# Kernel tuning notes

Hardware: AMD Instinct MI355X
Metric: run time of the kernel (lower is better)

Reference implementation:

```python
import jax, jax.numpy as jnp
import numpy as np

DT = 0.01
T, D_IN, D_STATE = 262144, 64, 128

def setup_inputs() -> dict:
    key = jax.random.key(0)
    k1, k2, k3, k4 = jax.random.split(key, 4)
    U = jax.random.normal(k1, (T, D_IN), dtype=jnp.float32)
    A_log = jax.random.normal(k2, (D_STATE,), dtype=jnp.float32) * 0.1 - 1.0
    B = jax.random.normal(k3, (D_STATE, D_IN), dtype=jnp.float32) * 0.1
    C = jax.random.normal(k4, (D_IN, D_STATE), dtype=jnp.float32) * 0.1
    Dm = jnp.zeros((D_IN, D_IN), dtype=jnp.float32)
    h0 = jnp.zeros((D_STATE,), dtype=jnp.float32)
    return {"U": U, "A_log": A_log, "B": B, "C": C, "D": Dm, "h0": h0}

def reference(U, A_log, B, C, D, h0):
    # Discretized diagonal transition: A_disc = exp(A_log * dt)
    A_d = jnp.exp(A_log * DT)  # (d_state,)
    Bu = U @ B.T               # (T, d_state), precompute all input injections
    Du = U @ D.T               # (T, d_input)

    def step(h, bu):
        h_new = A_d * h + bu
        return h_new, h_new

    h_final, H = jax.lax.scan(step, h0, Bu)  # H: (T, d_state)
    Y = H @ C.T + Du                          # (T, d_input)
    return Y, h_final
```

## Files before the change

### kernel.cpp

```cpp
#include <hip/hip_runtime.h>


#define TT   262144
#define DIN  64
#define DS   128
#define DTC  0.01f
#define L    128
#define NG   (TT / L)
#define SEGL 16
#define NSEG (NG / SEGL)

typedef short  s8v  __attribute__((ext_vector_type(8)));
typedef float  f4v  __attribute__((ext_vector_type(4)));

__device__ __forceinline__ unsigned short f2bf(float f) {
    unsigned u = __float_as_uint(f);
    u += 0x7fffu + ((u >> 16) & 1u);
    return (unsigned short)(u >> 16);
}

__device__ __forceinline__ s8v pack8(float4 a, float4 b) {
    union { unsigned short u[8]; s8v v; } r;
    r.u[0] = f2bf(a.x); r.u[1] = f2bf(a.y); r.u[2] = f2bf(a.z); r.u[3] = f2bf(a.w);
    r.u[4] = f2bf(b.x); r.u[5] = f2bf(b.y); r.u[6] = f2bf(b.z); r.u[7] = f2bf(b.w);
    return r.v;
}

__device__ __forceinline__ const s8v* afrag(const unsigned short* sA,
                                            int mt, int ks, int q, int m) {
    int slot = (mt * 2 + ks) * 64 + (q << 4) + (m ^ (q << 2) ^ ks);
    return (const s8v*)&sA[slot * 8];
}

__device__ __forceinline__ void stage_U(const float* __restrict__ Ug,
                                        unsigned short* __restrict__ sA,
                                        int tid) {
    #pragma unroll
    for (int p = 0; p < 2; ++p) {
        int u  = tid + p * 512;
        int mt = u >> 7, ks = (u >> 6) & 1, q = (u >> 4) & 3, lo = u & 15;
        int m  = lo ^ (q << 2) ^ ks;
        const float4* gp = (const float4*)(Ug + (mt * 16 + m) * DIN + ks * 32 + q * 8);
        *(s8v*)&sA[u * 8] = pack8(gp[0], gp[1]);
    }
}

__device__ __forceinline__ s8v load_bfrag(const float* __restrict__ M,
                                          int row, int k0, int ld) {
    const float4* p = (const float4*)(M + row * ld + k0);
    return pack8(p[0], p[1]);
}

__global__ __launch_bounds__(512, 8) void ssm_k1(
    const float* __restrict__ U, const float* __restrict__ Alog,
    const float* __restrict__ B, float* __restrict__ agg,
    float* __restrict__ segAgg)
{
    __shared__ __align__(16) unsigned short sA[8192];
    const int g    = blockIdx.x;
    const int tid  = threadIdx.x;
    const int lane = tid & 63;
    const int w    = tid >> 6;
    const int q    = lane >> 4, m = lane & 15;
    const int s    = 16 * w + m;

    stage_U(U + (size_t)g * L * DIN, sA, tid);

    s8v Bf[2];
    #pragma unroll
    for (int ks = 0; ks < 2; ++ks)
        Bf[ks] = load_bfrag(B, s, ks * 32 + q * 8, DIN);

    const float cA   = Alog[s] * DTC;
    const float aInv = __expf(-cA);
    __syncthreads();

    float wsum = 0.f;
    #pragma unroll
    for (int mt = 0; mt < 8; ++mt) {
        f4v acc = (f4v){0.f, 0.f, 0.f, 0.f};
        #pragma unroll
        for (int ks = 0; ks < 2; ++ks)
            acc = __builtin_amdgcn_mfma_f32_16x16x32_bf16(*afrag(sA, mt, ks, q, m), Bf[ks], acc, 0, 0, 0);
        float wb = __expf(cA * (float)(L - 1 - (mt * 16 + q * 4)));
        #pragma unroll
        for (int r = 0; r < 4; ++r) {
            wsum = fmaf(wb, acc[r], wsum);
            if (r < 3) wb *= aInv;
        }
    }
    wsum += __shfl_xor(wsum, 16, 64);
    wsum += __shfl_xor(wsum, 32, 64);

    if (q == 0) {
        agg[(size_t)g * DS + s] = wsum;
        float wgt = __expf(cA * (float)(L * (SEGL - 1 - (g & (SEGL - 1)))));
        atomicAdd(&segAgg[(g >> 4) * DS + s], wsum * wgt);
    }
}

__global__ void ssm_k2(const float* __restrict__ Alog, const float* __restrict__ h0,
                       const float* __restrict__ segAgg, float* __restrict__ segCarry,
                       float* __restrict__ hfin)
{
    const int s = threadIdx.x;
    const float aSeg = __expf(Alog[s] * (DTC * L * SEGL));
    float c = h0[s];
    #pragma unroll 8
    for (int sg = 0; sg < NSEG; ++sg) {
        segCarry[sg * DS + s] = c;
        c = fmaf(aSeg, c, segAgg[sg * DS + s]);
    }
    hfin[s] = c;
}

__global__ __launch_bounds__(512, 6) void ssm_k3(
    const float* __restrict__ U, const float* __restrict__ Alog,
    const float* __restrict__ B, const float* __restrict__ C,
    const float* __restrict__ Dm, const float* __restrict__ agg,
    const float* __restrict__ segCarry, float* __restrict__ Y)
{
    __shared__ __align__(16) unsigned short sA[8192];
    __shared__ __align__(16) float sBu[64 * 130];
    unsigned short* sHb = (unsigned short*)sBu;

    const int g    = blockIdx.x;
    const int tid  = threadIdx.x;
    const int lane = tid & 63;
    const int w    = tid >> 6;
    const int q    = lane >> 4, m = lane & 15;
    const int iC   = 16 * (w & 3) + m;

    stage_U(U + (size_t)g * L * DIN, sA, tid);

    s8v Bf[2], Cf[4], Df[2];
    #pragma unroll
    for (int ks = 0; ks < 2; ++ks)
        Bf[ks] = load_bfrag(B, 16 * w + m, ks * 32 + q * 8, DIN);
    #pragma unroll
    for (int ks = 0; ks < 4; ++ks)
        Cf[ks] = load_bfrag(C, iC, ks * 32 + q * 8, DS);
    #pragma unroll
    for (int ks = 0; ks < 2; ++ks)
        Df[ks] = load_bfrag(Dm, iC, ks * 32 + q * 8, DIN);

    float a_s = 0.f, hreg = 0.f;
    if (tid < DS) {
        const float cA  = Alog[tid] * DTC;
        a_s = __expf(cA);
        const float caL = cA * (float)L;
        const float aL  = __expf(caL);
        const int   j   = g & (SEGL - 1);
        const int   gb  = g & ~(SEGL - 1);
        float c0 = segCarry[(g >> 4) * DS + tid] * __expf(caL * (float)j);
        float wt = 1.f;
        for (int c = j - 1; c >= 0; --c) {
            c0 = fmaf(wt, agg[(size_t)(gb + c) * DS + tid], c0);
            wt *= aL;
        }
        hreg = c0;
    }
    __syncthreads();

    #pragma unroll
    for (int hh = 0; hh < 2; ++hh) {
        #pragma unroll
        for (int mtl = 0; mtl < 4; ++mtl) {
            f4v acc = (f4v){0.f, 0.f, 0.f, 0.f};
            const int mt = hh * 4 + mtl;
            #pragma unroll
            for (int ks = 0; ks < 2; ++ks)
                acc = __builtin_amdgcn_mfma_f32_16x16x32_bf16(*afrag(sA, mt, ks, q, m), Bf[ks], acc, 0, 0, 0);
            #pragma unroll
            for (int r = 0; r < 4; ++r)
                sBu[(mtl * 16 + q * 4 + r) * 130 + 16 * w + m] = acc[r];
        }
        __syncthreads();

        if (tid < DS) {
            #pragma unroll
            for (int r = 0; r < 64; ++r) {
                hreg = fmaf(a_s, hreg, sBu[r * 130 + tid]);
                sBu[r * 130 + tid] = hreg;
            }
        }
        __syncthreads();

        float4 pr[2][2];
        int tt[2], cc[2];
        #pragma unroll
        for (int p = 0; p < 2; ++p) {
            int u  = tid + p * 512;
            int t  = (u & 3) + ((u >> 6) << 2);
            int c8 = (u >> 2) & 15;
            tt[p] = t; cc[p] = c8;
            const float4* hp = (const float4*)&sBu[t * 130 + c8 * 8];
            pr[p][0] = hp[0]; pr[p][1] = hp[1];
        }
        __syncthreads();
        #pragma unroll
        for (int p = 0; p < 2; ++p) {
            int t = tt[p], c8 = cc[p];
            int mth = t >> 4, mm = t & 15, ks4 = c8 >> 2, qq = c8 & 3;
            int slot = mth * 256 + ks4 * 64 + qq * 16 + (mm ^ (qq << 2) ^ ks4);
            *(s8v*)&sHb[slot * 8] = pack8(pr[p][0], pr[p][1]);
        }
        __syncthreads();

        const int mm2 = w >> 2;
        #pragma unroll
        for (int ti = 0; ti < 2; ++ti) {
            const int mtl = mm2 * 2 + ti;
            f4v acc2 = (f4v){0.f, 0.f, 0.f, 0.f};
            #pragma unroll
            for (int ks = 0; ks < 4; ++ks) {
                int slot = mtl * 256 + ks * 64 + q * 16 + (m ^ (q << 2) ^ ks);
                acc2 = __builtin_amdgcn_mfma_f32_16x16x32_bf16(*(const s8v*)&sHb[slot * 8], Cf[ks], acc2, 0, 0, 0);
            }
            #pragma unroll
            for (int ks = 0; ks < 2; ++ks)
                acc2 = __builtin_amdgcn_mfma_f32_16x16x32_bf16(*afrag(sA, hh * 4 + mtl, ks, q, m), Df[ks], acc2, 0, 0, 0);
            const size_t tb = (size_t)g * L + hh * 64 + mtl * 16 + q * 4;
            #pragma unroll
            for (int r = 0; r < 4; ++r)
                Y[(tb + r) * DIN + iC] = acc2[r];
        }
        __syncthreads();
    }
}

extern "C" void kernel_launch(void* const* d_in, const int* in_sizes, int n_in,
                              void* d_out, int out_size, void* d_ws, size_t ws_size,
                              hipStream_t stream)
{
    const float* U    = (const float*)d_in[0];
    const float* Alog = (const float*)d_in[1];
    const float* B    = (const float*)d_in[2];
    const float* C    = (const float*)d_in[3];
    const float* Dm   = (const float*)d_in[4];
    const float* h0   = (const float*)d_in[5];

    float* out  = (float*)d_out;
    float* Yp   = out;
    float* hfin = out + (size_t)TT * DIN;

    float* agg      = (float*)d_ws;
    float* segAgg   = agg + (size_t)NG * DS;
    float* segCarry = segAgg + (size_t)NSEG * DS;

    hipMemsetAsync(segAgg, 0, (size_t)NSEG * DS * sizeof(float), stream);
    ssm_k1<<<NG, 512, 0, stream>>>(U, Alog, B, agg, segAgg);
    ssm_k2<<<1, DS, 0, stream>>>(Alog, h0, segAgg, segCarry, hfin);
    ssm_k3<<<NG, 512, 0, stream>>>(U, Alog, B, C, Dm, agg, segCarry, Yp);
}
```

Measured before the change: 214.3 us.

## Replace in-block serial scan with MFMA triangular prefix and flatten carry chain

```diff
diff --git a/kernel.cpp b/kernel.cpp
--- a/kernel.cpp
+++ b/kernel.cpp
@@ -7,10 +7,9 @@
 #define DTC  0.01f
 #define L    128
 #define NG   (TT / L)
-#define SEGL 16
-#define NSEG (NG / SEGL)
 
 typedef short  s8v  __attribute__((ext_vector_type(8)));
+typedef short  s4v  __attribute__((ext_vector_type(4)));
 typedef float  f4v  __attribute__((ext_vector_type(4)));
 
 __device__ __forceinline__ unsigned short f2bf(float f) {
@@ -26,10 +25,19 @@
     return r.v;
 }
 
-__device__ __forceinline__ const s8v* afrag(const unsigned short* sA,
-                                            int mt, int ks, int q, int m) {
-    int slot = (mt * 2 + ks) * 64 + (q << 4) + (m ^ (q << 2) ^ ks);
-    return (const s8v*)&sA[slot * 8];
+__device__ __forceinline__ s4v pack4(float x, float y, float z, float w) {
+    union { unsigned short u[4]; s4v v; } r;
+    r.u[0] = f2bf(x); r.u[1] = f2bf(y); r.u[2] = f2bf(z); r.u[3] = f2bf(w);
+    return r.v;
+}
+
+__device__ __forceinline__ int gidx(int NCO, int rtile, int co, int mf) {
+    return (((rtile * NCO + co) << 4) + (mf ^ (co & 15))) << 3;
+}
+
+__device__ __forceinline__ s8v ldfrag(const unsigned short* S, int NCO,
+                                      int rtile, int kt, int q, int m) {
+    return *(const s8v*)&S[gidx(NCO, rtile, kt * 4 + q, m)];
 }
 
 __device__ __forceinline__ void stage_U(const float* __restrict__ Ug,
@@ -38,10 +46,9 @@
     #pragma unroll
     for (int p = 0; p < 2; ++p) {
         int u  = tid + p * 512;
-        int mt = u >> 7, ks = (u >> 6) & 1, q = (u >> 4) & 3, lo = u & 15;
-        int m  = lo ^ (q << 2) ^ ks;
-        const float4* gp = (const float4*)(Ug + (mt * 16 + m) * DIN + ks * 32 + q * 8);
-        *(s8v*)&sA[u * 8] = pack8(gp[0], gp[1]);
+        int co = u & 7, m = (u >> 3) & 15, mt = u >> 7;
+        const float4* gp = (const float4*)(Ug + (mt * 16 + m) * DIN + co * 8);
+        *(s8v*)&sA[gidx(8, mt, co, m)] = pack8(gp[0], gp[1]);
     }
 }
 
@@ -51,10 +58,9 @@
     return pack8(p[0], p[1]);
 }
 
-__global__ __launch_bounds__(512, 8) void ssm_k1(
+__global__ __launch_bounds__(512, 4) void ssm_k1(
     const float* __restrict__ U, const float* __restrict__ Alog,
-    const float* __restrict__ B, float* __restrict__ agg,
-    float* __restrict__ segAgg)
+    const float* __restrict__ B, float* __restrict__ agg)
 {
     __shared__ __align__(16) unsigned short sA[8192];
     const int g    = blockIdx.x;
@@ -71,45 +77,44 @@
     for (int ks = 0; ks < 2; ++ks)
         Bf[ks] = load_bfrag(B, s, ks * 32 + q * 8, DIN);
 
-    const float cA   = Alog[s] * DTC;
-    const float aInv = __expf(-cA);
-    __syncthreads();
-
+    const float cA = Alog[s] * DTC;
+    __syncthreads();
+
+    float ainv = __expf(-cA);
+    float a16i = __expf(-16.f * cA);
+    float wmt  = __expf(cA * (float)(127 - 4 * q));
     float wsum = 0.f;
     #pragma unroll
     for (int mt = 0; mt < 8; ++mt) {
         f4v acc = (f4v){0.f, 0.f, 0.f, 0.f};
         #pragma unroll
         for (int ks = 0; ks < 2; ++ks)
-            acc = __builtin_amdgcn_mfma_f32_16x16x32_bf16(*afrag(sA, mt, ks, q, m), Bf[ks], acc, 0, 0, 0);
-        float wb = __expf(cA * (float)(L - 1 - (mt * 16 + q * 4)));
+            acc = __builtin_amdgcn_mfma_f32_16x16x32_bf16(
+                ldfrag(sA, 8, mt, ks, q, m), Bf[ks], acc, 0, 0, 0);
+        float wr = wmt;
         #pragma unroll
         for (int r = 0; r < 4; ++r) {
-            wsum = fmaf(wb, acc[r], wsum);
-            if (r < 3) wb *= aInv;
-        }
+            wsum = fmaf(wr, acc[r], wsum);
+            wr *= ainv;
+        }
+        wmt *= a16i;
     }
     wsum += __shfl_xor(wsum, 16, 64);
     wsum += __shfl_xor(wsum, 32, 64);
-
-    if (q == 0) {
-        agg[(size_t)g * DS + s] = wsum;
-        float wgt = __expf(cA * (float)(L * (SEGL - 1 - (g & (SEGL - 1)))));
-        atomicAdd(&segAgg[(g >> 4) * DS + s], wsum * wgt);
-    }
+    if (q == 0) agg[(size_t)g * DS + s] = wsum;
 }
 
 __global__ void ssm_k2(const float* __restrict__ Alog, const float* __restrict__ h0,
-                       const float* __restrict__ segAgg, float* __restrict__ segCarry,
-                       float* __restrict__ hfin)
+                       float* agg, float* __restrict__ hfin)
 {
     const int s = threadIdx.x;
-    const float aSeg = __expf(Alog[s] * (DTC * L * SEGL));
+    const float aL = __expf(Alog[s] * (DTC * (float)L));
     float c = h0[s];
     #pragma unroll 8
-    for (int sg = 0; sg < NSEG; ++sg) {
-        segCarry[sg * DS + s] = c;
-        c = fmaf(aSeg, c, segAgg[sg * DS + s]);
+    for (int g = 0; g < NG; ++g) {
+        float v = agg[(size_t)g * DS + s];
+        agg[(size_t)g * DS + s] = c;
+        c = fmaf(aL, c, v);
     }
     hfin[s] = c;
 }
@@ -117,115 +122,131 @@
 __global__ __launch_bounds__(512, 6) void ssm_k3(
     const float* __restrict__ U, const float* __restrict__ Alog,
     const float* __restrict__ B, const float* __restrict__ C,
-    const float* __restrict__ Dm, const float* __restrict__ agg,
-    const float* __restrict__ segCarry, float* __restrict__ Y)
+    const float* __restrict__ Dm, const float* __restrict__ carry,
+    float* __restrict__ Y)
 {
     __shared__ __align__(16) unsigned short sA[8192];
-    __shared__ __align__(16) float sBu[64 * 130];
-    unsigned short* sHb = (unsigned short*)sBu;
+    __shared__ __align__(16) unsigned short sT[16384];
+    __shared__ float sCA[DS];
+    __shared__ float sDc[DS];
 
     const int g    = blockIdx.x;
     const int tid  = threadIdx.x;
     const int lane = tid & 63;
     const int w    = tid >> 6;
     const int q    = lane >> 4, m = lane & 15;
-    const int iC   = 16 * (w & 3) + m;
-
-    stage_U(U + (size_t)g * L * DIN, sA, tid);
-
-    s8v Bf[2], Cf[4], Df[2];
+
+    s8v Bf[2];
     #pragma unroll
     for (int ks = 0; ks < 2; ++ks)
         Bf[ks] = load_bfrag(B, 16 * w + m, ks * 32 + q * 8, DIN);
-    #pragma unroll
-    for (int ks = 0; ks < 4; ++ks)
-        Cf[ks] = load_bfrag(C, iC, ks * 32 + q * 8, DS);
-    #pragma unroll
-    for (int ks = 0; ks < 2; ++ks)
-        Df[ks] = load_bfrag(Dm, iC, ks * 32 + q * 8, DIN);
-
-    float a_s = 0.f, hreg = 0.f;
+    const float cA = Alog[16 * w + m] * DTC;
+
+    stage_U(U + (size_t)g * L * DIN, sA, tid);
     if (tid < DS) {
-        const float cA  = Alog[tid] * DTC;
-        a_s = __expf(cA);
-        const float caL = cA * (float)L;
-        const float aL  = __expf(caL);
-        const int   j   = g & (SEGL - 1);
-        const int   gb  = g & ~(SEGL - 1);
-        float c0 = segCarry[(g >> 4) * DS + tid] * __expf(caL * (float)j);
-        float wt = 1.f;
-        for (int c = j - 1; c >= 0; --c) {
-            c0 = fmaf(wt, agg[(size_t)(gb + c) * DS + tid], c0);
-            wt *= aL;
-        }
-        hreg = c0;
-    }
-    __syncthreads();
-
-    #pragma unroll
-    for (int hh = 0; hh < 2; ++hh) {
-        #pragma unroll
-        for (int mtl = 0; mtl < 4; ++mtl) {
+        float ca = Alog[tid] * DTC;
+        sCA[tid] = ca;
+        sDc[tid] = __expf(ca) * carry[(size_t)g * DS + tid];
+    }
+    __syncthreads();
+
+    {
+        float ainv = __expf(-cA);
+        float a16i = __expf(-16.f * cA);
+        float fmt  = __expf(-cA * (float)(4 * q));
+        #pragma unroll
+        for (int mt = 0; mt < 8; ++mt) {
             f4v acc = (f4v){0.f, 0.f, 0.f, 0.f};
-            const int mt = hh * 4 + mtl;
             #pragma unroll
             for (int ks = 0; ks < 2; ++ks)
-                acc = __builtin_amdgcn_mfma_f32_16x16x32_bf16(*afrag(sA, mt, ks, q, m), Bf[ks], acc, 0, 0, 0);
+                acc = __builtin_amdgcn_mfma_f32_16x16x32_bf16(
+                    ldfrag(sA, 8, mt, ks, q, m), Bf[ks], acc, 0, 0, 0);
+            float f0 = fmt, f1 = f0 * ainv, f2 = f1 * ainv, f3 = f2 * ainv;
+            s4v pk = pack4(acc[0] * f0, acc[1] * f1, acc[2] * f2, acc[3] * f3);
+            *(s4v*)&sT[gidx(16, w, mt * 2 + (q >> 1), m) + (q & 1) * 4] = pk;
+            fmt *= a16i;
+        }
+    }
+    __syncthreads();
+
+    const int KBmax = w >> 1;
+    const int thr   = m + 16 * (w & 1);
+    s8v ones, part;
+    {
+        union { unsigned short u[8]; s8v v; } o, p;
+        #pragma unroll
+        for (int j = 0; j < 8; ++j) {
+            o.u[j] = 0x3F80;
+            p.u[j] = (q * 8 + j <= thr) ? 0x3F80 : 0;
+        }
+        ones = o.v; part = p.v;
+    }
+    const float tf = (float)(16 * w + m);
+    s4v pk[8];
+    #pragma unroll
+    for (int grp = 0; grp < 2; ++grp) {
+        f4v acc[4];
+        #pragma unroll
+        for (int i = 0; i < 4; ++i) acc[i] = (f4v){0.f, 0.f, 0.f, 0.f};
+        for (int kb = 0; kb <= KBmax; ++kb) {
+            s8v bfr = (kb < KBmax) ? ones : part;
             #pragma unroll
-            for (int r = 0; r < 4; ++r)
-                sBu[(mtl * 16 + q * 4 + r) * 130 + 16 * w + m] = acc[r];
-        }
-        __syncthreads();
-
-        if (tid < DS) {
-            #pragma unroll
-            for (int r = 0; r < 64; ++r) {
-                hreg = fmaf(a_s, hreg, sBu[r * 130 + tid]);
-                sBu[r * 130 + tid] = hreg;
-            }
-        }
-        __syncthreads();
-
-        float4 pr[2][2];
-        int tt[2], cc[2];
-        #pragma unroll
-        for (int p = 0; p < 2; ++p) {
-            int u  = tid + p * 512;
-            int t  = (u & 3) + ((u >> 6) << 2);
-            int c8 = (u >> 2) & 15;
-            tt[p] = t; cc[p] = c8;
-            const float4* hp = (const float4*)&sBu[t * 130 + c8 * 8];
-            pr[p][0] = hp[0]; pr[p][1] = hp[1];
-        }
-        __syncthreads();
-        #pragma unroll
-        for (int p = 0; p < 2; ++p) {
-            int t = tt[p], c8 = cc[p];
-            int mth = t >> 4, mm = t & 15, ks4 = c8 >> 2, qq = c8 & 3;
-            int slot = mth * 256 + ks4 * 64 + qq * 16 + (mm ^ (qq << 2) ^ ks4);
-            *(s8v*)&sHb[slot * 8] = pack8(pr[p][0], pr[p][1]);
-        }
-        __syncthreads();
-
-        const int mm2 = w >> 2;
-        #pragma unroll
-        for (int ti = 0; ti < 2; ++ti) {
-            const int mtl = mm2 * 2 + ti;
-            f4v acc2 = (f4v){0.f, 0.f, 0.f, 0.f};
-            #pragma unroll
-            for (int ks = 0; ks < 4; ++ks) {
-                int slot = mtl * 256 + ks * 64 + q * 16 + (m ^ (q << 2) ^ ks);
-                acc2 = __builtin_amdgcn_mfma_f32_16x16x32_bf16(*(const s8v*)&sHb[slot * 8], Cf[ks], acc2, 0, 0, 0);
-            }
-            #pragma unroll
-            for (int ks = 0; ks < 2; ++ks)
-                acc2 = __builtin_amdgcn_mfma_f32_16x16x32_bf16(*afrag(sA, hh * 4 + mtl, ks, q, m), Df[ks], acc2, 0, 0, 0);
-            const size_t tb = (size_t)g * L + hh * 64 + mtl * 16 + q * 4;
-            #pragma unroll
-            for (int r = 0; r < 4; ++r)
-                Y[(tb + r) * DIN + iC] = acc2[r];
-        }
-        __syncthreads();
+            for (int msl = 0; msl < 4; ++msl)
+                acc[msl] = __builtin_amdgcn_mfma_f32_16x16x32_bf16(
+                    ldfrag(sT, 16, grp * 4 + msl, kb, q, m), bfr, acc[msl], 0, 0, 0);
+        }
+        #pragma unroll
+        for (int msl = 0; msl < 4; ++msl) {
+            const int ms = grp * 4 + msl;
+            const float4 cav = *(const float4*)&sCA[16 * ms + 4 * q];
+            const float4 dcv = *(const float4*)&sDc[16 * ms + 4 * q];
+            pk[grp * 4 + msl] = pack4(
+                __expf(cav.x * tf) * (acc[msl][0] + dcv.x),
+                __expf(cav.y * tf) * (acc[msl][1] + dcv.y),
+                __expf(cav.z * tf) * (acc[msl][2] + dcv.z),
+                __expf(cav.w * tf) * (acc[msl][3] + dcv.w));
+        }
+    }
+
+    const int mi = w & 3, th = w >> 2;
+    float4 craw[4][2], draw[2][2];
+    #pragma unroll
+    for (int ks = 0; ks < 4; ++ks) {
+        const float4* p = (const float4*)(C + (16 * mi + m) * DS + ks * 32 + q * 8);
+        craw[ks][0] = p[0]; craw[ks][1] = p[1];
+    }
+    #pragma unroll
+    for (int ks = 0; ks < 2; ++ks) {
+        const float4* p = (const float4*)(Dm + (16 * mi + m) * DIN + ks * 32 + q * 8);
+        draw[ks][0] = p[0]; draw[ks][1] = p[1];
+    }
+
+    __syncthreads();
+    #pragma unroll
+    for (int ms = 0; ms < 8; ++ms)
+        *(s4v*)&sT[gidx(16, w, ms * 2 + (q >> 1), m) + (q & 1) * 4] = pk[ms];
+    __syncthreads();
+
+    s8v Cf[4], Df[2];
+    #pragma unroll
+    for (int ks = 0; ks < 4; ++ks) Cf[ks] = pack8(craw[ks][0], craw[ks][1]);
+    #pragma unroll
+    for (int ks = 0; ks < 2; ++ks) Df[ks] = pack8(draw[ks][0], draw[ks][1]);
+
+    float* Yb = Y + (size_t)g * L * DIN;
+    #pragma unroll
+    for (int nn = 0; nn < 4; ++nn) {
+        const int nt2 = th * 4 + nn;
+        f4v acc2 = (f4v){0.f, 0.f, 0.f, 0.f};
+        #pragma unroll
+        for (int ks = 0; ks < 4; ++ks)
+            acc2 = __builtin_amdgcn_mfma_f32_16x16x32_bf16(
+                Cf[ks], ldfrag(sT, 16, nt2, ks, q, m), acc2, 0, 0, 0);
+        #pragma unroll
+        for (int ks = 0; ks < 2; ++ks)
+            acc2 = __builtin_amdgcn_mfma_f32_16x16x32_bf16(
+                Df[ks], ldfrag(sA, 8, nt2, ks, q, m), acc2, 0, 0, 0);
+        *(f4v*)(Yb + (16 * nt2 + m) * DIN + 16 * mi + 4 * q) = acc2;
     }
 }
 
@@ -244,12 +265,9 @@
     float* Yp   = out;
     float* hfin = out + (size_t)TT * DIN;
 
-    float* agg      = (float*)d_ws;
-    float* segAgg   = agg + (size_t)NG * DS;
-    float* segCarry = segAgg + (size_t)NSEG * DS;
-
-    hipMemsetAsync(segAgg, 0, (size_t)NSEG * DS * sizeof(float), stream);
-    ssm_k1<<<NG, 512, 0, stream>>>(U, Alog, B, agg, segAgg);
-    ssm_k2<<<1, DS, 0, stream>>>(Alog, h0, segAgg, segCarry, hfin);
-    ssm_k3<<<NG, 512, 0, stream>>>(U, Alog, B, C, Dm, agg, segCarry, Yp);
-}
+    float* agg = (float*)d_ws;
+
+    ssm_k1<<<NG, 512, 0, stream>>>(U, Alog, B, agg);
+    ssm_k2<<<1, DS, 0, stream>>>(Alog, h0, agg, hfin);
+    ssm_k3<<<NG, 512, 0, stream>>>(U, Alog, B, C, Dm, agg, Yp);
+}
```

After: 301.2 us. 1.41x slower.
